# Kernel tuning notes

Hardware: AMD Instinct MI355X
Metric: run time of the kernel (lower is better)

## Reference

```python
import jax, jax.numpy as jnp
import numpy as np

N_QUBITS = 4
N_LAYERS = 2
PI = np.float32(np.pi)


def _rot_mat(phi, theta, omega):
    """PennyLane Rot(phi, theta, omega) = RZ(omega) RY(theta) RZ(phi), 2x2 complex."""
    c = jnp.cos(theta / 2).astype(jnp.complex64)
    s = jnp.sin(theta / 2).astype(jnp.complex64)
    ep = jnp.exp(-1j * (phi + omega) / 2).astype(jnp.complex64)  # e^{-i(phi+omega)/2}
    em = jnp.exp(-1j * (phi - omega) / 2).astype(jnp.complex64)  # e^{-i(phi-omega)/2}
    row0 = jnp.stack([ep * c, -jnp.conj(em) * s])
    row1 = jnp.stack([em * s, jnp.conj(ep) * c])
    return jnp.stack([row0, row1])  # (2,2)


def _apply_1q(psi, mat, wire):
    # psi: (N,2,2,2,2), wire axis = wire+1 (wire 0 is MSB, PennyLane convention)
    ax = wire + 1
    x = jnp.moveaxis(psi, ax, -1)
    x = x @ mat.T  # out[..., a] = sum_b mat[a,b] x[..., b]
    return jnp.moveaxis(x, -1, ax)


def _apply_cnot(psi, ctrl, tgt):
    cax, tax = ctrl + 1, tgt + 1
    p0 = jax.lax.index_in_dim(psi, 0, cax, keepdims=True)
    p1 = jnp.flip(jax.lax.index_in_dim(psi, 1, cax, keepdims=True), axis=tax)
    return jnp.concatenate([p0, p1], axis=cax)


def _quantum_features(patches, weights):
    """patches: (N,4) in [0,1]; weights: (L,4,3). Returns (N,4) PauliZ expvals."""
    # Encoding: RX(x*pi) then RY(x*pi) on |0> per wire -> product state.
    half = patches.astype(jnp.float32) * (PI / 2)  # half-angles
    c = jnp.cos(half)
    s = jnp.sin(half)
    # RY(a) @ RX(a) @ |0> = [c^2 + i s^2,  s c - i c s]
    v0 = (c * c) + 1j * (s * s)
    v1 = (s * c) - 1j * (c * s)
    v = jnp.stack([v0, v1], axis=-1).astype(jnp.complex64)  # (N, 4 wires, 2)
    psi = jnp.einsum('na,nb,nc,nd->nabcd', v[:, 0], v[:, 1], v[:, 2], v[:, 3])  # (N,2,2,2,2)

    n_layers = weights.shape[0]
    for l in range(n_layers):
        for w in range(N_QUBITS):
            psi = _apply_1q(psi, _rot_mat(weights[l, w, 0], weights[l, w, 1], weights[l, w, 2]), w)
        r = l % (N_QUBITS - 1) + 1  # StronglyEntanglingLayers default ranges
        for w in range(N_QUBITS):
            psi = _apply_cnot(psi, w, (w + r) % N_QUBITS)

    probs = (psi.real ** 2 + psi.imag ** 2).reshape(-1, 2 ** N_QUBITS)  # (N,16)
    # Z signs: wire 0 is most-significant bit of the state index
    bits = (jnp.arange(16)[:, None] >> jnp.arange(N_QUBITS - 1, -1, -1)[None, :]) & 1
    signs = (1.0 - 2.0 * bits).astype(probs.dtype)  # (16,4)
    return probs @ signs  # (N,4)


def setup_inputs() -> dict:
    key = jax.random.key(0)
    k1, k2 = jax.random.split(key)
    x = jax.random.uniform(k1, (32, 224, 224, 1), dtype=jnp.float32)  # grayscale in [0,1]
    weights = jax.random.uniform(k2, (N_LAYERS, N_QUBITS, 3), dtype=jnp.float32) * (2 * PI)
    return {"x": x, "weights": weights}


def reference(x, weights):
    B, H, W = x.shape[0], x.shape[1], x.shape[2]
    oh, ow = H // 2, W // 2
    # 2x2 patch extraction exactly as in the original call()
    p = x[..., 0].reshape(B, oh, 2, ow, 2).transpose(0, 1, 3, 2, 4).reshape(-1, 4)
    feats = _quantum_features(p, weights)
    return feats.reshape(B, oh, ow, N_QUBITS)
```

## Files before the change

### kernel.cpp

```cpp
#include <hip/hip_runtime.h>

#define N_PATCH (32 * 112 * 112)

__global__ __launch_bounds__(256) void qfeat_kernel(const float* __restrict__ x,
                                                    const float* __restrict__ wts,
                                                    float* __restrict__ out) {
    __shared__ __align__(16) float4 gs[19];
    __shared__ __align__(16) float4 nv[4];

    if (threadIdx.x < 4) {
        const int w = threadIdx.x;
        float phi = wts[w*3+0], th = wts[w*3+1], om = wts[w*3+2];
        float sP,cP,sT,cT,sO,cO;
        sincosf(phi,&sP,&cP); sincosf(th,&sT,&cT); sincosf(om,&sO,&cO);
        float r00 = cO*cT*cP - sO*sP, r01 = -cO*cT*sP - sO*cP, r02 = cO*sT;
        float r10 = sO*cT*cP + cO*sP, r11 = -sO*cT*sP + cO*cP, r12 = sO*sT;
        float r20 = -sT*cP,           r21 =  sT*sP,            r22 = cT;
        gs[3*w+0] = make_float4(r00, r10, r20, 0.f);
        gs[3*w+1] = make_float4(-r01, -r11, -r21, 0.f);
        gs[3*w+2] = make_float4(r02, r12, r22, 0.f);
    } else if (threadIdx.x < 8) {
        const int v = threadIdx.x - 4;
        float phi = wts[(4+v)*3+0], th = wts[(4+v)*3+1];
        float sP,cP,sT,cT;
        sincosf(phi,&sP,&cP); sincosf(th,&sT,&cT);
        nv[v] = make_float4(-sT*cP, sT*sP, cT, 0.f);
    }
    __syncthreads();
    if (threadIdx.x == 0) {
        float4 n0 = nv[0], n1 = nv[1], n2 = nv[2], n3 = nv[3];
        gs[12] = make_float4(n2.x, n2.y, n2.z, 0.f);
        gs[13] = make_float4(n3.x, -n3.y, n3.z, 0.f);
        gs[14] = make_float4( n0.x*n2.x, -n0.x*n2.y, -n0.x*n2.z, -n0.y*n2.x);
        gs[15] = make_float4( n0.y*n2.y,  n0.y*n2.z, -n0.z*n2.x,  n0.z*n2.y);
        gs[16] = make_float4( n0.z*n2.z,  n1.x*n3.x, -n1.x*n3.y, -n1.x*n3.z);
        gs[17] = make_float4( n1.y*n3.x,  n1.y*n3.y,  n1.y*n3.z, -n1.z*n3.x);
        gs[18] = make_float4( n1.z*n3.y,  n1.z*n3.z, 0.f, 0.f);
    }
    __syncthreads();

    const int pid = blockIdx.x * 256 + threadIdx.x;
    int j = pid % 112;
    int t = pid / 112;
    int i = t % 112;
    int b = t / 112;

    const float2 top = *reinterpret_cast<const float2*>(x + (((size_t)b * 224 + 2 * i) * 224 + 2 * j));
    const float2 bot = *reinterpret_cast<const float2*>(x + (((size_t)b * 224 + 2 * i + 1) * 224 + 2 * j));
    float p[4] = {top.x, top.y, bot.x, bot.y};

    float mx[4], my[4], mz[4];
#pragma unroll
    for (int w = 0; w < 4; ++w) {
        float S = __builtin_amdgcn_sinf(0.5f * p[w]);
        float C = __builtin_amdgcn_cosf(0.5f * p[w]);
        float e0 = S * C, e2 = C * C;
        float4 c0 = gs[3*w], c1 = gs[3*w+1], c2 = gs[3*w+2];
        mx[w] = c0.x * e0 + c1.x * S + c2.x * e2;
        my[w] = c0.y * e0 + c1.y * S + c2.y * e2;
        mz[w] = c0.z * e0 + c1.z * S + c2.z * e2;
    }

    float4 A = gs[12], B = gs[13];
    float4 c14 = gs[14], c15 = gs[15], c16 = gs[16], c17 = gs[17], c18 = gs[18];

    float x01 = mx[0]*mx[1], y01 = my[0]*my[1], z01 = mz[0]*mz[1];
    float x23 = mx[2]*mx[3], y23 = my[2]*my[3], z23 = mz[2]*mz[3];
    float y2x3 = my[2]*mx[3];

    float o0 = A.x*x23 + A.y*(z01*y2x3) + A.z*(z01*mz[2]);
    float o1 = B.x*(x01*mx[3]) + B.y*(y01*(mz[2]*my[3])) + B.z*(z01*z23);
    float o2 = c14.x*(x01*x23) + c14.y*(y01*y2x3) + c14.z*(y01*mz[2]) + c14.w*(mx[0]*my[1]*y23)
             + c15.x*(my[0]*mx[1]*mx[2]*my[3]) + c15.y*(my[0]*mx[1]*mz[3]) + c15.z*(mz[1]*y23)
             + c15.w*(mz[0]*mx[2]*my[3]) + c16.x*(mz[0]*mz[3]);
    float o3 = c16.y*(mx[0]*x23) + c16.z*(my[0]*mz[1]*y23) + c16.w*(mz[0]*my[1]*my[2]*mz[3])
             + c17.x*(my[0]*mz[1]*x23) + c17.y*(mx[0]*y23) + c17.z*(mx[1]*my[2]*mz[3])
             + c17.w*(y01*mx[3]) + c18.x*(x01*mz[2]*my[3]) + c18.y*z23;

    *reinterpret_cast<float4*>(out + (size_t)pid * 4) = make_float4(o0, o1, o2, o3);
}

extern "C" void kernel_launch(void* const* d_in, const int* in_sizes, int n_in,
                              void* d_out, int out_size, void* d_ws, size_t ws_size,
                              hipStream_t stream) {
    const float* x   = (const float*)d_in[0];
    const float* wts = (const float*)d_in[1];
    float* out       = (float*)d_out;
    qfeat_kernel<<<N_PATCH / 256, 256, 0, stream>>>(x, wts, out);
}
```

Measured before the change: 11.90 us.

## Overlap input loads with weight setup, drop second barrier, use 512-thread blocks

Issues the global loads of each thread's 2x2 patch before the per-block weight preprocessing, so memory latency overlaps the setup. The products of the second-layer coefficients are no longer precomputed into shared memory by one thread behind a second barrier. Each thread now factors o2 and o3 as dot products with the raw second-layer vectors. Setup sincosf calls are replaced by hardware sin/cos intrinsics on revolution-scaled angles, and blocks grow to 512 threads so the setup runs half as often; the cost is a few extra multiplies per thread and possible precision loss for large angles.

```diff
diff --git a/kernel.cpp b/kernel.cpp
--- a/kernel.cpp
+++ b/kernel.cpp
@@ -1,45 +1,12 @@
 #include <hip/hip_runtime.h>
 
 #define N_PATCH (32 * 112 * 112)
+#define TPB 512
 
-__global__ __launch_bounds__(256) void qfeat_kernel(const float* __restrict__ x,
+__global__ __launch_bounds__(TPB) void qfeat_kernel(const float* __restrict__ x,
                                                     const float* __restrict__ wts,
                                                     float* __restrict__ out) {
-    __shared__ __align__(16) float4 gs[19];
-    __shared__ __align__(16) float4 nv[4];
-
-    if (threadIdx.x < 4) {
-        const int w = threadIdx.x;
-        float phi = wts[w*3+0], th = wts[w*3+1], om = wts[w*3+2];
-        float sP,cP,sT,cT,sO,cO;
-        sincosf(phi,&sP,&cP); sincosf(th,&sT,&cT); sincosf(om,&sO,&cO);
-        float r00 = cO*cT*cP - sO*sP, r01 = -cO*cT*sP - sO*cP, r02 = cO*sT;
-        float r10 = sO*cT*cP + cO*sP, r11 = -sO*cT*sP + cO*cP, r12 = sO*sT;
-        float r20 = -sT*cP,           r21 =  sT*sP,            r22 = cT;
-        gs[3*w+0] = make_float4(r00, r10, r20, 0.f);
-        gs[3*w+1] = make_float4(-r01, -r11, -r21, 0.f);
-        gs[3*w+2] = make_float4(r02, r12, r22, 0.f);
-    } else if (threadIdx.x < 8) {
-        const int v = threadIdx.x - 4;
-        float phi = wts[(4+v)*3+0], th = wts[(4+v)*3+1];
-        float sP,cP,sT,cT;
-        sincosf(phi,&sP,&cP); sincosf(th,&sT,&cT);
-        nv[v] = make_float4(-sT*cP, sT*sP, cT, 0.f);
-    }
-    __syncthreads();
-    if (threadIdx.x == 0) {
-        float4 n0 = nv[0], n1 = nv[1], n2 = nv[2], n3 = nv[3];
-        gs[12] = make_float4(n2.x, n2.y, n2.z, 0.f);
-        gs[13] = make_float4(n3.x, -n3.y, n3.z, 0.f);
-        gs[14] = make_float4( n0.x*n2.x, -n0.x*n2.y, -n0.x*n2.z, -n0.y*n2.x);
-        gs[15] = make_float4( n0.y*n2.y,  n0.y*n2.z, -n0.z*n2.x,  n0.z*n2.y);
-        gs[16] = make_float4( n0.z*n2.z,  n1.x*n3.x, -n1.x*n3.y, -n1.x*n3.z);
-        gs[17] = make_float4( n1.y*n3.x,  n1.y*n3.y,  n1.y*n3.z, -n1.z*n3.x);
-        gs[18] = make_float4( n1.z*n3.y,  n1.z*n3.z, 0.f, 0.f);
-    }
-    __syncthreads();
-
-    const int pid = blockIdx.x * 256 + threadIdx.x;
+    const int pid = blockIdx.x * TPB + threadIdx.x;
     int j = pid % 112;
     int t = pid / 112;
     int i = t % 112;
@@ -47,6 +14,34 @@
 
     const float2 top = *reinterpret_cast<const float2*>(x + (((size_t)b * 224 + 2 * i) * 224 + 2 * j));
     const float2 bot = *reinterpret_cast<const float2*>(x + (((size_t)b * 224 + 2 * i + 1) * 224 + 2 * j));
+
+    __shared__ __align__(16) float4 gcol[12];
+    __shared__ __align__(16) float4 nv[4];
+
+    if (threadIdx.x < 8) {
+        const float INV2PI = 0.15915494309189535f;
+        if (threadIdx.x < 4) {
+            const int w = threadIdx.x;
+            float phi = wts[w*3+0], th = wts[w*3+1], om = wts[w*3+2];
+            float sP = __builtin_amdgcn_sinf(phi*INV2PI), cP = __builtin_amdgcn_cosf(phi*INV2PI);
+            float sT = __builtin_amdgcn_sinf(th *INV2PI), cT = __builtin_amdgcn_cosf(th *INV2PI);
+            float sO = __builtin_amdgcn_sinf(om *INV2PI), cO = __builtin_amdgcn_cosf(om *INV2PI);
+            float r00 = cO*cT*cP - sO*sP, r01 = -cO*cT*sP - sO*cP, r02 = cO*sT;
+            float r10 = sO*cT*cP + cO*sP, r11 = -sO*cT*sP + cO*cP, r12 = sO*sT;
+            float r20 = -sT*cP,           r21 =  sT*sP,            r22 = cT;
+            gcol[3*w+0] = make_float4(r00, r10, r20, 0.f);
+            gcol[3*w+1] = make_float4(-r01, -r11, -r21, 0.f);
+            gcol[3*w+2] = make_float4(r02, r12, r22, 0.f);
+        } else {
+            const int v = threadIdx.x - 4;
+            float phi = wts[(4+v)*3+0], th = wts[(4+v)*3+1];
+            float sP = __builtin_amdgcn_sinf(phi*INV2PI), cP = __builtin_amdgcn_cosf(phi*INV2PI);
+            float sT = __builtin_amdgcn_sinf(th *INV2PI), cT = __builtin_amdgcn_cosf(th *INV2PI);
+            nv[v] = make_float4(-sT*cP, sT*sP, cT, 0.f);
+        }
+    }
+    __syncthreads();
+
     float p[4] = {top.x, top.y, bot.x, bot.y};
 
     float mx[4], my[4], mz[4];
@@ -55,27 +50,28 @@
         float S = __builtin_amdgcn_sinf(0.5f * p[w]);
         float C = __builtin_amdgcn_cosf(0.5f * p[w]);
         float e0 = S * C, e2 = C * C;
-        float4 c0 = gs[3*w], c1 = gs[3*w+1], c2 = gs[3*w+2];
+        float4 c0 = gcol[3*w], c1 = gcol[3*w+1], c2 = gcol[3*w+2];
         mx[w] = c0.x * e0 + c1.x * S + c2.x * e2;
         my[w] = c0.y * e0 + c1.y * S + c2.y * e2;
         mz[w] = c0.z * e0 + c1.z * S + c2.z * e2;
     }
 
-    float4 A = gs[12], B = gs[13];
-    float4 c14 = gs[14], c15 = gs[15], c16 = gs[16], c17 = gs[17], c18 = gs[18];
+    float4 n0 = nv[0], n1 = nv[1], n2 = nv[2], n3 = nv[3];
 
     float x01 = mx[0]*mx[1], y01 = my[0]*my[1], z01 = mz[0]*mz[1];
     float x23 = mx[2]*mx[3], y23 = my[2]*my[3], z23 = mz[2]*mz[3];
     float y2x3 = my[2]*mx[3];
 
-    float o0 = A.x*x23 + A.y*(z01*y2x3) + A.z*(z01*mz[2]);
-    float o1 = B.x*(x01*mx[3]) + B.y*(y01*(mz[2]*my[3])) + B.z*(z01*z23);
-    float o2 = c14.x*(x01*x23) + c14.y*(y01*y2x3) + c14.z*(y01*mz[2]) + c14.w*(mx[0]*my[1]*y23)
-             + c15.x*(my[0]*mx[1]*mx[2]*my[3]) + c15.y*(my[0]*mx[1]*mz[3]) + c15.z*(mz[1]*y23)
-             + c15.w*(mz[0]*mx[2]*my[3]) + c16.x*(mz[0]*mz[3]);
-    float o3 = c16.y*(mx[0]*x23) + c16.z*(my[0]*mz[1]*y23) + c16.w*(mz[0]*my[1]*my[2]*mz[3])
-             + c17.x*(my[0]*mz[1]*x23) + c17.y*(mx[0]*y23) + c17.z*(mx[1]*my[2]*mz[3])
-             + c17.w*(y01*mx[3]) + c18.x*(x01*mz[2]*my[3]) + c18.y*z23;
+    float o0 = n2.x*x23 + n2.y*(z01*y2x3) + n2.z*(z01*mz[2]);
+    float o1 = n3.x*(x01*mx[3]) - n3.y*(y01*(mz[2]*my[3])) + n3.z*(z01*z23);
+    float ix =  n2.x*(x01*x23)          - n2.y*(y01*y2x3)           - n2.z*(y01*mz[2]);
+    float iy = -n2.x*(mx[0]*my[1]*y23)  + n2.y*(my[0]*mx[1]*mx[2]*my[3]) + n2.z*(my[0]*mx[1]*mz[3]);
+    float iz = -n2.x*(mz[1]*y23)        + n2.y*(mz[0]*mx[2]*my[3])  + n2.z*(mz[0]*mz[3]);
+    float o2 = n0.x*ix + n0.y*iy + n0.z*iz;
+    float jx =  n3.x*(mx[0]*x23)        - n3.y*(my[0]*mz[1]*y23)    - n3.z*(mz[0]*my[1]*my[2]*mz[3]);
+    float jy =  n3.x*(my[0]*mz[1]*x23)  + n3.y*(mx[0]*y23)          + n3.z*(mx[1]*my[2]*mz[3]);
+    float jz = -n3.x*(y01*mx[3])        + n3.y*(x01*mz[2]*my[3])    + n3.z*z23;
+    float o3 = n1.x*jx + n1.y*jy + n1.z*jz;
 
     *reinterpret_cast<float4*>(out + (size_t)pid * 4) = make_float4(o0, o1, o2, o3);
 }
@@ -86,5 +82,5 @@
     const float* x   = (const float*)d_in[0];
     const float* wts = (const float*)d_in[1];
     float* out       = (float*)d_out;
-    qfeat_kernel<<<N_PATCH / 256, 256, 0, stream>>>(x, wts, out);
+    qfeat_kernel<<<N_PATCH / TPB, TPB, 0, stream>>>(x, wts, out);
 }
```

After: 10.56 us. -11.3%, faster.
